# Optimization experiments

Measured on AMD Instinct MI355X. Metric: run time of the kernel, lower is better.

The kernel has to match this reference:

```python
import jax, jax.numpy as jnp
import numpy as np


def _warp(input1, input2):
    """Bilinear flow warp. input1: [B,C,H,W] features, input2: [B,2,H,W] flow (dx,dy).
    Out-of-bounds samples contribute zero (matches typical warp_cuda kernels)."""
    B, C, H, W = input1.shape
    # sample coordinates: x = j + flow_x, y = i + flow_y
    gy, gx = jnp.meshgrid(jnp.arange(H, dtype=input1.dtype),
                          jnp.arange(W, dtype=input1.dtype), indexing='ij')
    x = gx[None] + input2[:, 0]  # [B,H,W]
    y = gy[None] + input2[:, 1]

    x0 = jnp.floor(x)
    y0 = jnp.floor(y)
    x1 = x0 + 1.0
    y1 = y0 + 1.0
    # bilinear weights
    wx1 = x - x0
    wx0 = 1.0 - wx1
    wy1 = y - y0
    wy0 = 1.0 - wy1

    img = jnp.transpose(input1, (0, 2, 3, 1))  # [B,H,W,C], channels-last for gather
    bidx = jnp.arange(B)[:, None, None]        # [B,1,1]

    def sample(yy, xx):
        # zero outside bounds
        valid = (yy >= 0) & (yy <= H - 1) & (xx >= 0) & (xx <= W - 1)
        yi = jnp.clip(yy, 0, H - 1).astype(jnp.int32)
        xi = jnp.clip(xx, 0, W - 1).astype(jnp.int32)
        v = img[bidx, yi, xi]  # [B,H,W,C]
        return v * valid[..., None].astype(img.dtype)

    out = (sample(y0, x0) * (wy0 * wx0)[..., None]
           + sample(y0, x1) * (wy0 * wx1)[..., None]
           + sample(y1, x0) * (wy1 * wx0)[..., None]
           + sample(y1, x1) * (wy1 * wx1)[..., None])  # [B,H,W,C]
    return jnp.transpose(out, (0, 3, 1, 2))  # [B,C,H,W]


def setup_inputs() -> dict:
    key = jax.random.key(0)
    k1, k2 = jax.random.split(key)
    B, C, H, W = 8, 64, 256, 448
    input1 = jax.random.normal(k1, (B, C, H, W), dtype=jnp.float32)
    # flow of a few pixels magnitude
    input2 = jax.random.normal(k2, (B, 2, H, W), dtype=jnp.float32) * 4.0
    return {"input1": input1, "input2": input2}


def reference(input1, input2):
    return _warp(input1, input2)
```

## Files before the change

kernel.cpp:

```cpp
#include <hip/hip_runtime.h>

constexpr int B = 8, C = 64, H = 256, W = 448;
constexpr int HW = H * W;
constexpr int NPIX = B * HW;
constexpr int BLK = 256;
constexpr int XCDS = 8;

constexpr int NBLOCKS_V1 = NPIX / BLK;
constexpr int BLOCKS_PER_XCD_V1 = NBLOCKS_V1 / XCDS;

constexpr int TILE = 64;
constexpr int TILES_PER_ROW = W / TILE;
constexpr int TILES_PER_IMG = HW / TILE;
constexpr int NBLOCKS_V2 = B * TILES_PER_IMG;
constexpr int BLOCKS_PER_XCD_V2 = NBLOCKS_V2 / XCDS;
constexpr size_t WS_NEEDED = (size_t)B * HW * C * sizeof(float);

__global__ __launch_bounds__(256) void transpose_kernel(
    const float* __restrict__ img,
    float* __restrict__ tmp)
{
    __shared__ float lds[64][65];

    int blk = blockIdx.x;
    int b   = blk / TILES_PER_IMG;
    int t   = blk - b * TILES_PER_IMG;
    int hw0 = t * TILE;

    int pc = threadIdx.x & 15;
    int cg = threadIdx.x >> 4;
    const float* src = img + (size_t)b * C * HW + hw0 + 4 * pc;
    #pragma unroll
    for (int k = 0; k < 4; ++k) {
        int c = cg + 16 * k;
        float4 v = *(const float4*)(src + (size_t)c * HW);
        lds[c][4 * pc + 0] = v.x;
        lds[c][4 * pc + 1] = v.y;
        lds[c][4 * pc + 2] = v.z;
        lds[c][4 * pc + 3] = v.w;
    }
    __syncthreads();

    int lc = threadIdx.x & 15;
    int pg = threadIdx.x >> 4;
    float* dst = tmp + ((size_t)b * HW + hw0) * C + 4 * lc;
    #pragma unroll
    for (int k = 0; k < 4; ++k) {
        int px = pg + 16 * k;
        float4 v;
        v.x = lds[4 * lc + 0][px];
        v.y = lds[4 * lc + 1][px];
        v.z = lds[4 * lc + 2][px];
        v.w = lds[4 * lc + 3][px];
        *(float4*)(dst + (size_t)px * C) = v;
    }
}

__global__ __launch_bounds__(256) void gather_kernel(
    const float* __restrict__ tmp,
    const float* __restrict__ flow,
    float* __restrict__ out)
{
    __shared__ float sm[64][65];

    int bid = blockIdx.x;
    int swz = (bid % XCDS) * BLOCKS_PER_XCD_V2 + (bid / XCDS);

    int b  = swz / TILES_PER_IMG;
    int t  = swz - b * TILES_PER_IMG;
    int i  = t / TILES_PER_ROW;
    int j0 = (t - i * TILES_PER_ROW) * TILE;

    int lane = threadIdx.x & 63;
    int wv   = threadIdx.x >> 6;

    int pl = lane & 15;
    int p1 = wv * 16 + pl;
    int j  = j0 + p1;
    int ij = i * W + j;

    const float* fb = flow + (size_t)b * 2 * HW;
    float fx = fb[ij];
    float fy = fb[HW + ij];

    float x = (float)j + fx;
    float y = (float)i + fy;

    float x0f = floorf(x), y0f = floorf(y);
    int   x0  = (int)x0f,  y0  = (int)y0f;
    float wx1 = x - x0f,   wy1 = y - y0f;
    float wx0 = 1.0f - wx1, wy0 = 1.0f - wy1;

    bool vx0 = (x0 >= 0)  & (x0 <= W - 1);
    bool vx1 = (x0 >= -1) & (x0 <= W - 2);
    bool vy0 = (y0 >= 0)  & (y0 <= H - 1);
    bool vy1 = (y0 >= -1) & (y0 <= H - 2);

    float w00r = (vy0 & vx0) ? wy0 * wx0 : 0.0f;
    float w01r = (vy0 & vx1) ? wy0 * wx1 : 0.0f;
    float w10r = (vy1 & vx0) ? wy1 * wx0 : 0.0f;
    float w11r = (vy1 & vx1) ? wy1 * wx1 : 0.0f;

    int xi0 = min(max(x0, 0),     W - 1);
    int xi1 = min(max(x0 + 1, 0), W - 1);
    int yi0 = min(max(y0, 0),     H - 1);
    int yi1 = min(max(y0 + 1, 0), H - 1);

    int o00r = (yi0 * W + xi0) << 8;
    int o01r = (yi0 * W + xi1) << 8;
    int o10r = (yi1 * W + xi0) << 8;
    int o11r = (yi1 * W + xi1) << 8;

    const char* tb = (const char*)(tmp + (size_t)b * HW * C);

    #pragma unroll 4
    for (int pp = 0; pp < 16; ++pp) {
        int   o00 = __builtin_amdgcn_readlane(o00r, pp);
        int   o01 = __builtin_amdgcn_readlane(o01r, pp);
        int   o10 = __builtin_amdgcn_readlane(o10r, pp);
        int   o11 = __builtin_amdgcn_readlane(o11r, pp);
        float w00 = __int_as_float(__builtin_amdgcn_readlane(__float_as_int(w00r), pp));
        float w01 = __int_as_float(__builtin_amdgcn_readlane(__float_as_int(w01r), pp));
        float w10 = __int_as_float(__builtin_amdgcn_readlane(__float_as_int(w10r), pp));
        float w11 = __int_as_float(__builtin_amdgcn_readlane(__float_as_int(w11r), pp));

        const float* q00 = (const float*)(tb + (unsigned)o00);
        const float* q01 = (const float*)(tb + (unsigned)o01);
        const float* q10 = (const float*)(tb + (unsigned)o10);
        const float* q11 = (const float*)(tb + (unsigned)o11);

        float v00 = q00[lane];
        float v01 = q01[lane];
        float v10 = q10[lane];
        float v11 = q11[lane];

        float acc = w00 * v00 + w01 * v01 + w10 * v10 + w11 * v11;
        sm[lane][wv * 16 + pp] = acc;
    }
    __syncthreads();

    int pg = threadIdx.x & 15;
    int cg = threadIdx.x >> 4;
    float* ob = out + (size_t)b * C * HW + (size_t)i * W + j0 + 4 * pg;
    #pragma unroll
    for (int k = 0; k < 4; ++k) {
        int c = cg + 16 * k;
        float4 v;
        v.x = sm[c][4 * pg + 0];
        v.y = sm[c][4 * pg + 1];
        v.z = sm[c][4 * pg + 2];
        v.w = sm[c][4 * pg + 3];
        *(float4*)(ob + (size_t)c * HW) = v;
    }
}

__global__ __launch_bounds__(256) void warp_kernel(
    const float* __restrict__ img,
    const float* __restrict__ flow,
    float* __restrict__ out)
{
    int bid = blockIdx.x;
    int swz = (bid % XCDS) * BLOCKS_PER_XCD_V1 + (bid / XCDS);
    int pix = swz * BLK + threadIdx.x;

    int b  = pix / HW;
    int ij = pix - b * HW;
    int i  = ij / W;
    int j  = ij - i * W;

    float fx = flow[(size_t)(b * 2 + 0) * HW + ij];
    float fy = flow[(size_t)(b * 2 + 1) * HW + ij];

    float x = (float)j + fx;
    float y = (float)i + fy;

    float x0f = floorf(x), y0f = floorf(y);
    int   x0  = (int)x0f,  y0  = (int)y0f;
    float wx1 = x - x0f,   wy1 = y - y0f;
    float wx0 = 1.0f - wx1, wy0 = 1.0f - wy1;

    bool vx0 = (x0 >= 0)  & (x0 <= W - 1);
    bool vx1 = (x0 >= -1) & (x0 <= W - 2);
    bool vy0 = (y0 >= 0)  & (y0 <= H - 1);
    bool vy1 = (y0 >= -1) & (y0 <= H - 2);

    float w00 = (vy0 & vx0) ? wy0 * wx0 : 0.0f;
    float w01 = (vy0 & vx1) ? wy0 * wx1 : 0.0f;
    float w10 = (vy1 & vx0) ? wy1 * wx0 : 0.0f;
    float w11 = (vy1 & vx1) ? wy1 * wx1 : 0.0f;

    int xi0 = min(max(x0, 0),     W - 1);
    int xi1 = min(max(x0 + 1, 0), W - 1);
    int yi0 = min(max(y0, 0),     H - 1);
    int yi1 = min(max(y0 + 1, 0), H - 1);

    int o00 = yi0 * W + xi0;
    int o01 = yi0 * W + xi1;
    int o10 = yi1 * W + xi0;
    int o11 = yi1 * W + xi1;

    const float* ib = img + (size_t)b * C * HW;
    float*       ob = out + (size_t)b * C * HW + ij;

    #pragma unroll
    for (int cb = 0; cb < C; cb += 8) {
        float v00[8], v01[8], v10[8], v11[8];
        #pragma unroll
        for (int u = 0; u < 8; ++u) {
            const float* q = ib + (size_t)(cb + u) * HW;
            v00[u] = q[o00];
            v01[u] = q[o01];
            v10[u] = q[o10];
            v11[u] = q[o11];
        }
        #pragma unroll
        for (int u = 0; u < 8; ++u) {
            ob[(size_t)(cb + u) * HW] =
                w00 * v00[u] + w01 * v01[u] + w10 * v10[u] + w11 * v11[u];
        }
    }
}

extern "C" void kernel_launch(void* const* d_in, const int* in_sizes, int n_in,
                              void* d_out, int out_size, void* d_ws, size_t ws_size,
                              hipStream_t stream) {
    const float* img  = (const float*)d_in[0];
    const float* flow = (const float*)d_in[1];
    float* out = (float*)d_out;

    if (ws_size >= WS_NEEDED && d_ws != nullptr) {
        float* tmp = (float*)d_ws;
        transpose_kernel<<<dim3(NBLOCKS_V2), dim3(BLK), 0, stream>>>(img, tmp);
        gather_kernel<<<dim3(NBLOCKS_V2), dim3(BLK), 0, stream>>>(tmp, flow, out);
    } else {
        warp_kernel<<<dim3(NBLOCKS_V1), dim3(BLK), 0, stream>>>(img, flow, out);
    }
}
```

Before: 509.9 us.

## Widen transpose tiles to 128 pixels and batch gather loads via bpermute

The transpose kernel now handles 128 pixels per block, so each block writes one contiguous 32KB span of the channels-last buffer with fully coalesced float4 stores. The gather kernel replaces the readlane loop, which produced scalar per-pixel offsets, with ds_bpermute broadcasts. It also issues all 32 loads for 8 pixels before the math, to raise memory-level parallelism. This costs more VGPRs and moves the offsets into vector registers, which may turn scalar-base loads into per-lane addressed loads.

```diff
diff --git a/kernel.cpp b/kernel.cpp
--- a/kernel.cpp
+++ b/kernel.cpp
@@ -12,47 +12,53 @@
 constexpr int TILE = 64;
 constexpr int TILES_PER_ROW = W / TILE;
 constexpr int TILES_PER_IMG = HW / TILE;
-constexpr int NBLOCKS_V2 = B * TILES_PER_IMG;
-constexpr int BLOCKS_PER_XCD_V2 = NBLOCKS_V2 / XCDS;
+constexpr int NBLOCKS_G = B * TILES_PER_IMG;
+constexpr int BLOCKS_PER_XCD_G = NBLOCKS_G / XCDS;
 constexpr size_t WS_NEEDED = (size_t)B * HW * C * sizeof(float);
+
+constexpr int TP_PX = 128;
+constexpr int NBLOCKS_T = NPIX / TP_PX;
 
 __global__ __launch_bounds__(256) void transpose_kernel(
     const float* __restrict__ img,
     float* __restrict__ tmp)
 {
-    __shared__ float lds[64][65];
+    __shared__ float lds[64][129];
 
     int blk = blockIdx.x;
-    int b   = blk / TILES_PER_IMG;
-    int t   = blk - b * TILES_PER_IMG;
-    int hw0 = t * TILE;
-
-    int pc = threadIdx.x & 15;
-    int cg = threadIdx.x >> 4;
+    int b   = blk / (HW / TP_PX);
+    int t   = blk - b * (HW / TP_PX);
+    int hw0 = t * TP_PX;
+
+    int tid = threadIdx.x;
+    int pc  = tid & 15;
+    int cg  = tid >> 4;
+
     const float* src = img + (size_t)b * C * HW + hw0 + 4 * pc;
     #pragma unroll
-    for (int k = 0; k < 4; ++k) {
-        int c = cg + 16 * k;
-        float4 v = *(const float4*)(src + (size_t)c * HW);
-        lds[c][4 * pc + 0] = v.x;
-        lds[c][4 * pc + 1] = v.y;
-        lds[c][4 * pc + 2] = v.z;
-        lds[c][4 * pc + 3] = v.w;
+    for (int k = 0; k < 8; ++k) {
+        int c   = cg + 16 * (k & 3);
+        int px0 = 64 * (k >> 2);
+        float4 v = *(const float4*)(src + (size_t)c * HW + px0);
+        lds[c][px0 + 4 * pc + 0] = v.x;
+        lds[c][px0 + 4 * pc + 1] = v.y;
+        lds[c][px0 + 4 * pc + 2] = v.z;
+        lds[c][px0 + 4 * pc + 3] = v.w;
     }
     __syncthreads();
 
-    int lc = threadIdx.x & 15;
-    int pg = threadIdx.x >> 4;
-    float* dst = tmp + ((size_t)b * HW + hw0) * C + 4 * lc;
-    #pragma unroll
-    for (int k = 0; k < 4; ++k) {
-        int px = pg + 16 * k;
+    int lt = tid & 15;
+    int tg = tid >> 4;
+    float* dst = tmp + ((size_t)b * HW + hw0) * C;
+    #pragma unroll
+    for (int k = 0; k < 8; ++k) {
+        int px = 16 * k + tg;
         float4 v;
-        v.x = lds[4 * lc + 0][px];
-        v.y = lds[4 * lc + 1][px];
-        v.z = lds[4 * lc + 2][px];
-        v.w = lds[4 * lc + 3][px];
-        *(float4*)(dst + (size_t)px * C) = v;
+        v.x = lds[4 * lt + 0][px];
+        v.y = lds[4 * lt + 1][px];
+        v.z = lds[4 * lt + 2][px];
+        v.w = lds[4 * lt + 3][px];
+        *(float4*)(dst + k * 1024 + 4 * tid) = v;
     }
 }
 
@@ -64,15 +70,16 @@
     __shared__ float sm[64][65];
 
     int bid = blockIdx.x;
-    int swz = (bid % XCDS) * BLOCKS_PER_XCD_V2 + (bid / XCDS);
+    int swz = (bid % XCDS) * BLOCKS_PER_XCD_G + (bid / XCDS);
 
     int b  = swz / TILES_PER_IMG;
     int t  = swz - b * TILES_PER_IMG;
     int i  = t / TILES_PER_ROW;
     int j0 = (t - i * TILES_PER_ROW) * TILE;
 
-    int lane = threadIdx.x & 63;
-    int wv   = threadIdx.x >> 6;
+    int lane  = threadIdx.x & 63;
+    int wv    = threadIdx.x >> 6;
+    int lane4 = lane << 2;
 
     int pl = lane & 15;
     int p1 = wv * 16 + pl;
@@ -113,29 +120,32 @@
 
     const char* tb = (const char*)(tmp + (size_t)b * HW * C);
 
-    #pragma unroll 4
-    for (int pp = 0; pp < 16; ++pp) {
-        int   o00 = __builtin_amdgcn_readlane(o00r, pp);
-        int   o01 = __builtin_amdgcn_readlane(o01r, pp);
-        int   o10 = __builtin_amdgcn_readlane(o10r, pp);
-        int   o11 = __builtin_amdgcn_readlane(o11r, pp);
-        float w00 = __int_as_float(__builtin_amdgcn_readlane(__float_as_int(w00r), pp));
-        float w01 = __int_as_float(__builtin_amdgcn_readlane(__float_as_int(w01r), pp));
-        float w10 = __int_as_float(__builtin_amdgcn_readlane(__float_as_int(w10r), pp));
-        float w11 = __int_as_float(__builtin_amdgcn_readlane(__float_as_int(w11r), pp));
-
-        const float* q00 = (const float*)(tb + (unsigned)o00);
-        const float* q01 = (const float*)(tb + (unsigned)o01);
-        const float* q10 = (const float*)(tb + (unsigned)o10);
-        const float* q11 = (const float*)(tb + (unsigned)o11);
-
-        float v00 = q00[lane];
-        float v01 = q01[lane];
-        float v10 = q10[lane];
-        float v11 = q11[lane];
-
-        float acc = w00 * v00 + w01 * v01 + w10 * v10 + w11 * v11;
-        sm[lane][wv * 16 + pp] = acc;
+    #pragma unroll
+    for (int h = 0; h < 2; ++h) {
+        float vv[8][4];
+        #pragma unroll
+        for (int pp = 0; pp < 8; ++pp) {
+            int idx = (h * 8 + pp) << 2;
+            int o0 = __builtin_amdgcn_ds_bpermute(idx, o00r);
+            int o1 = __builtin_amdgcn_ds_bpermute(idx, o01r);
+            int o2 = __builtin_amdgcn_ds_bpermute(idx, o10r);
+            int o3 = __builtin_amdgcn_ds_bpermute(idx, o11r);
+            vv[pp][0] = *(const float*)(tb + (unsigned)(o0 + lane4));
+            vv[pp][1] = *(const float*)(tb + (unsigned)(o1 + lane4));
+            vv[pp][2] = *(const float*)(tb + (unsigned)(o2 + lane4));
+            vv[pp][3] = *(const float*)(tb + (unsigned)(o3 + lane4));
+        }
+        #pragma unroll
+        for (int pp = 0; pp < 8; ++pp) {
+            int idx = (h * 8 + pp) << 2;
+            float w0 = __int_as_float(__builtin_amdgcn_ds_bpermute(idx, __float_as_int(w00r)));
+            float w1 = __int_as_float(__builtin_amdgcn_ds_bpermute(idx, __float_as_int(w01r)));
+            float w2 = __int_as_float(__builtin_amdgcn_ds_bpermute(idx, __float_as_int(w10r)));
+            float w3 = __int_as_float(__builtin_amdgcn_ds_bpermute(idx, __float_as_int(w11r)));
+            float acc = w0 * vv[pp][0] + w1 * vv[pp][1]
+                      + w2 * vv[pp][2] + w3 * vv[pp][3];
+            sm[lane][wv * 16 + h * 8 + pp] = acc;
+        }
     }
     __syncthreads();
 
@@ -230,8 +240,8 @@
 
     if (ws_size >= WS_NEEDED && d_ws != nullptr) {
         float* tmp = (float*)d_ws;
-        transpose_kernel<<<dim3(NBLOCKS_V2), dim3(BLK), 0, stream>>>(img, tmp);
-        gather_kernel<<<dim3(NBLOCKS_V2), dim3(BLK), 0, stream>>>(tmp, flow, out);
+        transpose_kernel<<<dim3(NBLOCKS_T), dim3(BLK), 0, stream>>>(img, tmp);
+        gather_kernel<<<dim3(NBLOCKS_G), dim3(BLK), 0, stream>>>(tmp, flow, out);
     } else {
         warp_kernel<<<dim3(NBLOCKS_V1), dim3(BLK), 0, stream>>>(img, flow, out);
     }
```

After: 507.6 us. No clear change (-0.5%).
